# Performance work log

Measured on AMD Instinct MI355X. Metric: run time of the kernel, lower is better.

## Reference

```python
import jax, jax.numpy as jnp
import numpy as np

B, NV, NP, D, K = 8, 2048, 4096, 64, 8  # shapes per batch, vtx/pts counts, feat dim, num_interp
NEG = -1e9


def _unit(x):
    return x / jnp.clip(jnp.linalg.norm(x, axis=-1, keepdims=True), 1e-12)


def _gather(v, idx):
    # v: [B, N, C], idx: [B, Q, K] -> [B, Q, K, C]
    return jax.vmap(lambda a, i: a[i])(v, idx)


def setup_inputs() -> dict:
    key = jax.random.key(0)
    k1, k2, k3, k4, k5 = jax.random.split(key, 5)
    return {
        "vtx": jax.random.normal(k1, (B * NV, 3), jnp.float32),
        "pts": jax.random.normal(k2, (B * NP, 3), jnp.float32),
        "vtx_feature": jax.random.normal(k3, (B * NV, D), jnp.float32),
        "pts_feature": jax.random.normal(k4, (B * NP, D), jnp.float32),
        "vismask_logits": jax.random.normal(k5, (B * NV, 1), jnp.float32),
    }


def reference(vtx, pts, vtx_feature, pts_feature, vismask_logits):
    # --- per-batch min-max normalization of sigmoid(vismask) (serial loop in torch) ---
    vm = jax.nn.sigmoid(vismask_logits).reshape(B, NV, 1)
    vmin = vm.min(axis=1, keepdims=True)
    vmax = vm.max(axis=1, keepdims=True)
    vm = (vm - vmin) / (vmax - vmin)

    vtxb = vtx.reshape(B, NV, 3)
    ptsb = pts.reshape(B, NP, 3)
    vf = vtx_feature.reshape(B, NV, D)
    pf = pts_feature.reshape(B, NP, D)

    # --- cosine KNN: for each vtx, k nearest pts by cosine similarity ---
    sim = jnp.einsum('bnd,bmd->bnm', _unit(vf), _unit(pf))  # [B,NV,NP]
    _, idx = jax.lax.top_k(sim, K)                           # [B,NV,K]

    nbr_pts = _gather(ptsb, idx)                             # [B,NV,K,3]
    nbr_pf = _gather(pf, idx)                                # [B,NV,K,D]
    euclid = nbr_pts - vtxb[:, :, None, :]
    # raw (unnormalized) dot product, weighted by vismask of the query vertex
    fsim = jnp.sum(nbr_pf * vf[:, :, None, :], axis=-1, keepdims=True) * vm[:, :, None, :]
    # scatter_add over assign_index[0] == sum over the K grouped neighbors
    flow_init = jnp.sum(euclid * fsim, axis=2) / jnp.sum(fsim, axis=2)  # [B,NV,3]

    # --- interpolate flow at invisible vertices from visible ones (2nd cosine KNN) ---
    vis = vm >= 0.5                                          # [B,NV,1]
    vfn = _unit(vf)
    sim2 = jnp.einsum('bnd,bmd->bnm', vfn, vfn)              # [B,NV,NV]
    sim2 = jnp.where(vis[:, :, 0][:, None, :], sim2, NEG)    # keys restricted to visible vtx
    _, idx2 = jax.lax.top_k(sim2, K)                         # [B,NV,K]

    nbr_vf = _gather(vf, idx2)                               # [B,NV,K,D]
    nbr_flow = _gather(flow_init, idx2)                      # [B,NV,K,3]
    fsim2 = jnp.sum(nbr_vf * vf[:, :, None, :], axis=-1, keepdims=True)
    invis_flow = jnp.sum(nbr_flow * fsim2, axis=2) / jnp.sum(fsim2, axis=2)

    flow = jnp.where(vis, flow_init, invis_flow)             # flow_init[invis] = invis_flow
    l1_points = jnp.concatenate([flow, vm], axis=-1)         # [B,NV,4]
    return l1_points.reshape(B * NV, 4)
```

## Files before the change

kernel.cpp:

```cpp
#include <hip/hip_runtime.h>
#include <math.h>

#define BB 8
#define NVV 2048
#define NPP 4096
#define DD 64
#define NQ (BB * NVV)
#define QT (NQ / 16)
#define NC1 2
#define NC2 2

typedef __attribute__((ext_vector_type(8))) short short8;
typedef __attribute__((ext_vector_type(8))) unsigned short ushort8;
typedef __attribute__((ext_vector_type(4))) float f32x4;


__device__ __forceinline__ unsigned short bf16rn(float x) {
  unsigned u = __float_as_uint(x);
  return (unsigned short)((u + 0x7FFFu + ((u >> 16) & 1u)) >> 16);
}
__device__ __forceinline__ float bf2f(unsigned short h) {
  return __uint_as_float(((unsigned)h) << 16);
}

__device__ __forceinline__ void net8(unsigned* a, unsigned v) {
#pragma unroll
  for (int k = 0; k < 7; k++) {
    unsigned r;
    asm("v_med3_u32 %0, %1, %2, %3" : "=v"(r) : "v"(v), "v"(a[k]), "v"(a[k + 1]));
    a[k] = r;
  }
  a[7] = a[7] > v ? a[7] : v;
}

__device__ __forceinline__ void ins8(float* tv, int* ti, float v, int id) {
  bool c1 = v > tv[1], c2 = v > tv[2], c3 = v > tv[3];
  bool c4 = v > tv[4], c5 = v > tv[5], c6 = v > tv[6], c7 = v > tv[7];
  tv[0] = c1 ? tv[1] : v;                ti[0] = c1 ? ti[1] : id;
  tv[1] = c2 ? tv[2] : (c1 ? v : tv[1]); ti[1] = c2 ? ti[2] : (c1 ? id : ti[1]);
  tv[2] = c3 ? tv[3] : (c2 ? v : tv[2]); ti[2] = c3 ? ti[3] : (c2 ? id : ti[2]);
  tv[3] = c4 ? tv[4] : (c3 ? v : tv[3]); ti[3] = c4 ? ti[4] : (c3 ? id : ti[3]);
  tv[4] = c5 ? tv[5] : (c4 ? v : tv[4]); ti[4] = c5 ? ti[5] : (c4 ? id : ti[4]);
  tv[5] = c6 ? tv[6] : (c5 ? v : tv[5]); ti[5] = c6 ? ti[6] : (c5 ? id : ti[5]);
  tv[6] = c7 ? tv[7] : (c6 ? v : tv[6]); ti[6] = c7 ? ti[7] : (c6 ? id : ti[6]);
  tv[7] = c7 ? v : tv[7];                ti[7] = c7 ? id : ti[7];
}

__global__ __launch_bounds__(256) void k_prep(const float* __restrict__ logits,
                                              const float* __restrict__ vf,
                                              const float* __restrict__ pf,
                                              float* __restrict__ vm,
                                              float* __restrict__ inv_vf_s,
                                              float* __restrict__ inv_pf_s,
                                              unsigned short* __restrict__ vfh,
                                              unsigned short* __restrict__ vfl,
                                              unsigned short* __restrict__ pfh,
                                              unsigned short* __restrict__ pfl,
                                              float* __restrict__ out) {
  int bid = blockIdx.x, t = threadIdx.x;
  if (bid < BB) {
    int b = bid;
    __shared__ float smn[4], smx[4];
    float vals[8];
    float mn = 1e30f, mx = -1e30f;
#pragma unroll
    for (int i = 0; i < 8; i++) {
      float x = logits[b * NVV + t + i * 256];
      float s = 1.0f / (1.0f + expf(-x));
      vals[i] = s;
      mn = fminf(mn, s);
      mx = fmaxf(mx, s);
    }
    for (int o = 32; o; o >>= 1) {
      mn = fminf(mn, __shfl_xor(mn, o, 64));
      mx = fmaxf(mx, __shfl_xor(mx, o, 64));
    }
    int w = t >> 6;
    if ((t & 63) == 0) { smn[w] = mn; smx[w] = mx; }
    __syncthreads();
    mn = fminf(fminf(smn[0], smn[1]), fminf(smn[2], smn[3]));
    mx = fmaxf(fmaxf(smx[0], smx[1]), fmaxf(smx[2], smx[3]));
    float range = mx - mn;
#pragma unroll
    for (int i = 0; i < 8; i++) {
      float v = (vals[i] - mn) / range;
      int g = b * NVV + t + i * 256;
      vm[g] = v;
      out[g * 4 + 3] = v;
    }
  } else {
    int tile_g = (bid - BB) * 4 + (t >> 6);
    int lane = t & 63, c = lane & 15, quad = (lane >> 4) & 3;
    const float* src;
    unsigned short *dh, *dl;
    float* ginv;
    int tile;
    if (tile_g < QT) { tile = tile_g; src = vf; dh = vfh; dl = vfl; ginv = inv_vf_s; }
    else { tile = tile_g - QT; src = pf; dh = pfh; dl = pfl; ginv = inv_pf_s; }
    int row = tile * 16 + c;
    const float* rp = src + (size_t)row * DD + quad * 8;
    float4 a0 = *(const float4*)(rp);
    float4 b0 = *(const float4*)(rp + 4);
    float4 a1 = *(const float4*)(rp + 32);
    float4 b1 = *(const float4*)(rp + 36);
    float xs[16] = {a0.x, a0.y, a0.z, a0.w, b0.x, b0.y, b0.z, b0.w,
                    a1.x, a1.y, a1.z, a1.w, b1.x, b1.y, b1.z, b1.w};
    float ss = 0.f;
#pragma unroll
    for (int j = 0; j < 16; j++) ss = fmaf(xs[j], xs[j], ss);
    ss += __shfl_xor(ss, 16, 64);
    ss += __shfl_xor(ss, 32, 64);
    float inv = 1.0f / fmaxf(sqrtf(ss), 1e-12f);
    if (quad == 0) ginv[row] = 16384.0f * inv;
    ushort8 h, l;
    size_t s0 = (size_t)tile * 128 + lane;
#pragma unroll
    for (int j = 0; j < 8; j++) {
      float xn = xs[j] * inv;
      unsigned short hj = bf16rn(xn);
      h[j] = hj;
      l[j] = bf16rn(xn - bf2f(hj));
    }
    *(ushort8*)(dh + s0 * 8) = h;
    *(ushort8*)(dl + s0 * 8) = l;
#pragma unroll
    for (int j = 0; j < 8; j++) {
      float xn = xs[8 + j] * inv;
      unsigned short hj = bf16rn(xn);
      h[j] = hj;
      l[j] = bf16rn(xn - bf2f(hj));
    }
    *(ushort8*)(dh + (s0 + 64) * 8) = h;
    *(ushort8*)(dl + (s0 + 64) * 8) = l;
  }
}

__global__ __launch_bounds__(256)
void k_knn(const unsigned short* __restrict__ vfh, const unsigned short* __restrict__ vfl,
           const unsigned short* __restrict__ pfh, const unsigned short* __restrict__ pfl,
           const float* __restrict__ vm,
           unsigned* __restrict__ pc1, unsigned* __restrict__ pc2) {
  int wid = (blockIdx.x * 256 + threadIdx.x) >> 6;
  int lane = threadIdx.x & 63, col = lane & 15, quad = lane >> 4;

  const unsigned short *KH, *KL;
  const float* mask;
  unsigned* PC;
  int qt_g, bt0, row0, ckb, ntiles;
  if (wid < QT * NC1) {
    int ck = wid & 1;
    qt_g = wid >> 1;
    int batch = qt_g >> 7;
    KH = pfh; KL = pfl;
    mask = nullptr;
    ntiles = 128;
    bt0 = batch * 256 + ck * 128;
    PC = pc1;
    row0 = ck * 8; ckb = ck * 128;
  } else {
    int w = wid - QT * NC1;
    int ck = w & 1;
    qt_g = w >> 1;
    int batch = qt_g >> 7;
    KH = vfh; KL = vfl;
    mask = vm + batch * NVV;
    ntiles = 64;
    bt0 = batch * 128 + ck * 64;
    PC = pc2;
    row0 = ck * 8; ckb = ck * 64;
  }

  size_t ab = (size_t)qt_g * 1024 + lane * 8;
  short8 qh0 = *(const short8*)(vfh + ab);
  short8 qh1 = *(const short8*)(vfh + ab + 512);
  short8 ql0 = *(const short8*)(vfl + ab);
  short8 ql1 = *(const short8*)(vfl + ab + 512);
  asm volatile("" : "+a"(qh0), "+a"(qh1), "+a"(ql0), "+a"(ql1));

  unsigned tv[8];
#pragma unroll
  for (int k = 0; k < 8; k++) tv[k] = 0u;

#pragma unroll 2
  for (int kt = 0; kt < ntiles; kt++) {
    size_t bo = (size_t)(bt0 + kt) * 1024 + lane * 8;
    short8 kh0 = *(const short8*)(KH + bo);
    short8 kh1 = *(const short8*)(KH + bo + 512);
    short8 kl0 = *(const short8*)(KL + bo);
    short8 kl1 = *(const short8*)(KL + bo + 512);
    int base16 = (ckb + kt) * 16;
    f32x4 c = {0.f, 0.f, 0.f, 0.f};
    c = __builtin_amdgcn_mfma_f32_16x16x32_bf16(kh0, qh0, c, 0, 0, 0);
    c = __builtin_amdgcn_mfma_f32_16x16x32_bf16(kh1, qh1, c, 0, 0, 0);
    c = __builtin_amdgcn_mfma_f32_16x16x32_bf16(kh0, ql0, c, 0, 0, 0);
    c = __builtin_amdgcn_mfma_f32_16x16x32_bf16(kh1, ql1, c, 0, 0, 0);
    c = __builtin_amdgcn_mfma_f32_16x16x32_bf16(kl0, qh0, c, 0, 0, 0);
    c = __builtin_amdgcn_mfma_f32_16x16x32_bf16(kl1, qh1, c, 0, 0, 0);
    float4 mv;
    if (mask) mv = *(const float4*)(mask + base16 + quad * 4);
#pragma unroll
    for (int r = 0; r < 4; r++) {
      unsigned u = (unsigned)fmaxf(fmaf(c[r], 520000.0f, 520000.0f), 0.0f);
      unsigned pk = (u << 12) | (unsigned)(base16 + quad * 4 + r);
      if (mask) {
        float mr = (r == 0) ? mv.x : (r == 1) ? mv.y : (r == 2) ? mv.z : mv.w;
        pk = (mr >= 0.5f) ? pk : 0u;
      }
      net8(tv, pk);
    }
  }

#pragma unroll
  for (int m = 16; m <= 32; m <<= 1) {
    unsigned ov[8];
#pragma unroll
    for (int k = 0; k < 8; k++) ov[k] = (unsigned)__shfl_xor((int)tv[k], m, 64);
#pragma unroll
    for (int k = 7; k >= 0; k--) net8(tv, ov[k]);
  }

  if (quad == 0) {
    int q = qt_g * 16 + col;
#pragma unroll
    for (int k = 0; k < 8; k++)
      PC[(size_t)(row0 + k) * NQ + q] = tv[k];
  }
}

__device__ __forceinline__ float dot64(const float4* __restrict__ a,
                                       const float4* __restrict__ b) {
  float a0 = 0.f, a1 = 0.f, a2 = 0.f, a3 = 0.f;
#pragma unroll
  for (int c = 0; c < 16; c++) {
    float4 x = a[c], y = b[c];
    a0 = fmaf(x.x, y.x, a0);
    a1 = fmaf(x.y, y.y, a1);
    a2 = fmaf(x.z, y.z, a2);
    a3 = fmaf(x.w, y.w, a3);
  }
  return (a0 + a1) + (a2 + a3);
}

__global__ __launch_bounds__(256) void k_merge_flow(const unsigned* __restrict__ pc,
                                                    const float* __restrict__ vf,
                                                    const float* __restrict__ pf,
                                                    const float* __restrict__ pts,
                                                    const float* __restrict__ vtx,
                                                    const float* __restrict__ inv_pf_s,
                                                    float* __restrict__ flow_ws,
                                                    float* __restrict__ out) {
  int T = blockIdx.x * 256 + threadIdx.x;
  int q = T >> 4, c = T & 15, batch = q >> 11;
  const float4* qp = (const float4*)(vf + (size_t)q * DD);
  float tv[8];
  int ti[8];
#pragma unroll
  for (int k = 0; k < 8; k++) { tv[k] = -3.0e38f; ti[k] = 0; }
  {
    unsigned pk = pc[(size_t)c * NQ + q];
    int id = (int)(pk & 0xFFFu);
    int prow = batch * NPP + id;
    float s = dot64(qp, (const float4*)(pf + (size_t)prow * DD)) *
              inv_pf_s[prow] * 6.103515625e-5f;
    ins8(tv, ti, s, id);
  }
#pragma unroll
  for (int m = 1; m <= 8; m <<= 1) {
    float ov[8];
    int oi[8];
#pragma unroll
    for (int k = 0; k < 8; k++) {
      ov[k] = __shfl_xor(tv[k], m, 64);
      oi[k] = __shfl_xor(ti[k], m, 64);
    }
#pragma unroll
    for (int k = 7; k >= 0; k--)
      if (ov[k] > tv[0]) ins8(tv, ti, ov[k], oi[k]);
  }
  int id = ti[0];
  float sv = tv[0];
#pragma unroll
  for (int k = 1; k < 8; k++) {
    id = (c == k) ? ti[k] : id;
    sv = (c == k) ? tv[k] : sv;
  }

  float ax = 0.f, ay = 0.f, az = 0.f, den = 0.f;
  if (c < 8) {
    int prow = batch * NPP + id;
    float w = sv * 16384.0f / inv_pf_s[prow];
    ax = (pts[prow * 3 + 0] - vtx[q * 3 + 0]) * w;
    ay = (pts[prow * 3 + 1] - vtx[q * 3 + 1]) * w;
    az = (pts[prow * 3 + 2] - vtx[q * 3 + 2]) * w;
    den = w;
  }
#pragma unroll
  for (int m = 1; m <= 8; m <<= 1) {
    ax += __shfl_xor(ax, m, 64);
    ay += __shfl_xor(ay, m, 64);
    az += __shfl_xor(az, m, 64);
    den += __shfl_xor(den, m, 64);
  }
  if (c == 0) {
    float fx = ax / den, fy = ay / den, fz = az / den;
    flow_ws[q * 4 + 0] = fx;
    flow_ws[q * 4 + 1] = fy;
    flow_ws[q * 4 + 2] = fz;
    out[q * 4 + 0] = fx;
    out[q * 4 + 1] = fy;
    out[q * 4 + 2] = fz;
  }
}

__global__ __launch_bounds__(256) void k_merge_final(const unsigned* __restrict__ pc,
                                                     const float* __restrict__ vf,
                                                     const float* __restrict__ vm,
                                                     const float* __restrict__ inv_vf_s,
                                                     const float* __restrict__ flow_ws,
                                                     float* __restrict__ out) {
  int T = blockIdx.x * 256 + threadIdx.x;
  int q = T >> 4, c = T & 15, batch = q >> 11;
  if (vm[q] >= 0.5f) return;
  const float4* qp = (const float4*)(vf + (size_t)q * DD);
  float tv[8];
  int ti[8];
#pragma unroll
  for (int k = 0; k < 8; k++) { tv[k] = -3.0e38f; ti[k] = 0; }
  {
    unsigned pk = pc[(size_t)c * NQ + q];
    if (pk > 0xFFFu) {
      int id = (int)(pk & 0xFFFu);
      int krow = batch * NVV + id;
      float s = dot64(qp, (const float4*)(vf + (size_t)krow * DD)) *
                inv_vf_s[krow] * 6.103515625e-5f;
      ins8(tv, ti, s, id);
    }
  }
#pragma unroll
  for (int m = 1; m <= 8; m <<= 1) {
    float ov[8];
    int oi[8];
#pragma unroll
    for (int k = 0; k < 8; k++) {
      ov[k] = __shfl_xor(tv[k], m, 64);
      oi[k] = __shfl_xor(ti[k], m, 64);
    }
#pragma unroll
    for (int k = 7; k >= 0; k--)
      if (ov[k] > tv[0]) ins8(tv, ti, ov[k], oi[k]);
  }
  int id = ti[0];
  float sv = tv[0];
#pragma unroll
  for (int k = 1; k < 8; k++) {
    id = (c == k) ? ti[k] : id;
    sv = (c == k) ? tv[k] : sv;
  }

  float ax = 0.f, ay = 0.f, az = 0.f, den = 0.f;
  if (c < 8) {
    int krow = batch * NVV + id;
    float w = sv * 16384.0f / inv_vf_s[krow];
    ax = flow_ws[krow * 4 + 0] * w;
    ay = flow_ws[krow * 4 + 1] * w;
    az = flow_ws[krow * 4 + 2] * w;
    den = w;
  }
#pragma unroll
  for (int m = 1; m <= 8; m <<= 1) {
    ax += __shfl_xor(ax, m, 64);
    ay += __shfl_xor(ay, m, 64);
    az += __shfl_xor(az, m, 64);
    den += __shfl_xor(den, m, 64);
  }
  if (c == 0) {
    out[q * 4 + 0] = ax / den;
    out[q * 4 + 1] = ay / den;
    out[q * 4 + 2] = az / den;
  }
}

extern "C" void kernel_launch(void* const* d_in, const int* in_sizes, int n_in,
                              void* d_out, int out_size, void* d_ws, size_t ws_size,
                              hipStream_t stream) {
  const float* vtx = (const float*)d_in[0];
  const float* pts = (const float*)d_in[1];
  const float* vf = (const float*)d_in[2];
  const float* pf = (const float*)d_in[3];
  const float* lg = (const float*)d_in[4];
  float* out = (float*)d_out;
  float* ws = (float*)d_ws;

  float* vm = ws;
  float* inv_vf_s = ws + 16384;
  float* inv_pf_s = ws + 32768;
  float* flow = ws + 65536;
  unsigned* pc1 = (unsigned*)(ws + 131072);
  unsigned* pc2 = (unsigned*)(ws + 393216);
  unsigned short* vfh = (unsigned short*)(ws + 655360);
  unsigned short* vfl = (unsigned short*)(ws + 1179648);
  unsigned short* pfh = (unsigned short*)(ws + 1703936);
  unsigned short* pfl = (unsigned short*)(ws + 2752512);

  k_prep<<<BB + 768, 256, 0, stream>>>(lg, vf, pf, vm, inv_vf_s, inv_pf_s,
                                       vfh, vfl, pfh, pfl, out);
  k_knn<<<(QT * NC1 + QT * NC2) / 4, 256, 0, stream>>>(vfh, vfl, pfh, pfl,
                                                       vm, pc1, pc2);
  k_merge_flow<<<NQ * 16 / 256, 256, 0, stream>>>(pc1, vf, pf, pts, vtx,
                                                  inv_pf_s, flow, out);
  k_merge_final<<<NQ * 16 / 256, 256, 0, stream>>>(pc2, vf, vm, inv_vf_s, flow, out);
}
```

Before: 178.9 us.

## Split KNN key chunks across wave pairs and remap blocks per XCD

Each (query tile, key chunk) unit is now processed by two waves, each scanning half of the key tiles. The two partial top-8 lists are merged through shared memory after a block barrier. Block indices are also remapped so consecutive query tiles land on the same XCD, which should improve L2 reuse of key data. This doubles the wave count to shorten per-wave serial MFMA and sort chains, at the cost of an extra LDS merge and a __syncthreads.

Result: no change. 179.9 us (+0.6%).

```diff
diff --git a/kernel.cpp b/kernel.cpp
--- a/kernel.cpp
+++ b/kernel.cpp
@@ -140,34 +140,43 @@
            const unsigned short* __restrict__ pfh, const unsigned short* __restrict__ pfl,
            const float* __restrict__ vm,
            unsigned* __restrict__ pc1, unsigned* __restrict__ pc2) {
-  int wid = (blockIdx.x * 256 + threadIdx.x) >> 6;
-  int lane = threadIdx.x & 63, col = lane & 15, quad = lane >> 4;
+  __shared__ unsigned mg[2][16][8];
+
+  int p = blockIdx.x;
+  int tid = threadIdx.x;
+  int pairid = tid >> 7;
+  int wv = (tid >> 6) & 1;
+  int lane = tid & 63, col = lane & 15, quad = lane >> 4;
+
+  bool knn1 = p < 1024;
+  int q8 = knn1 ? p : (p - 1024);
+  int xcd = q8 & 7, idx = q8 >> 3;
+  int lb = xcd * 128 + idx;
+  int unit = lb * 2 + pairid;
+  int ck = unit & 1;
+  int qt_g = unit >> 1;
+  int batch = qt_g >> 7;
 
   const unsigned short *KH, *KL;
   const float* mask;
   unsigned* PC;
-  int qt_g, bt0, row0, ckb, ntiles;
-  if (wid < QT * NC1) {
-    int ck = wid & 1;
-    qt_g = wid >> 1;
-    int batch = qt_g >> 7;
+  int bt0, tilebase, half, row0;
+  if (knn1) {
     KH = pfh; KL = pfl;
     mask = nullptr;
-    ntiles = 128;
-    bt0 = batch * 256 + ck * 128;
+    half = 64;
+    bt0 = batch * 256 + ck * 128 + wv * 64;
+    tilebase = ck * 128 + wv * 64;
     PC = pc1;
-    row0 = ck * 8; ckb = ck * 128;
+    row0 = ck * 8;
   } else {
-    int w = wid - QT * NC1;
-    int ck = w & 1;
-    qt_g = w >> 1;
-    int batch = qt_g >> 7;
     KH = vfh; KL = vfl;
     mask = vm + batch * NVV;
-    ntiles = 64;
-    bt0 = batch * 128 + ck * 64;
+    half = 32;
+    bt0 = batch * 128 + ck * 64 + wv * 32;
+    tilebase = ck * 64 + wv * 32;
     PC = pc2;
-    row0 = ck * 8; ckb = ck * 64;
+    row0 = ck * 8;
   }
 
   size_t ab = (size_t)qt_g * 1024 + lane * 8;
@@ -182,13 +191,13 @@
   for (int k = 0; k < 8; k++) tv[k] = 0u;
 
 #pragma unroll 2
-  for (int kt = 0; kt < ntiles; kt++) {
+  for (int kt = 0; kt < half; kt++) {
     size_t bo = (size_t)(bt0 + kt) * 1024 + lane * 8;
     short8 kh0 = *(const short8*)(KH + bo);
     short8 kh1 = *(const short8*)(KH + bo + 512);
     short8 kl0 = *(const short8*)(KL + bo);
     short8 kl1 = *(const short8*)(KL + bo + 512);
-    int base16 = (ckb + kt) * 16;
+    int base16 = (tilebase + kt) * 16;
     f32x4 c = {0.f, 0.f, 0.f, 0.f};
     c = __builtin_amdgcn_mfma_f32_16x16x32_bf16(kh0, qh0, c, 0, 0, 0);
     c = __builtin_amdgcn_mfma_f32_16x16x32_bf16(kh1, qh1, c, 0, 0, 0);
@@ -219,8 +228,15 @@
     for (int k = 7; k >= 0; k--) net8(tv, ov[k]);
   }
 
-  if (quad == 0) {
-    int q = qt_g * 16 + col;
+  if (wv == 1 && lane < 16) {
+#pragma unroll
+    for (int k = 0; k < 8; k++) mg[pairid][lane][k] = tv[k];
+  }
+  __syncthreads();
+  if (wv == 0 && lane < 16) {
+#pragma unroll
+    for (int k = 0; k < 8; k++) net8(tv, mg[pairid][lane][k]);
+    int q = qt_g * 16 + lane;
 #pragma unroll
     for (int k = 0; k < 8; k++)
       PC[(size_t)(row0 + k) * NQ + q] = tv[k];
@@ -404,8 +420,7 @@
 
   k_prep<<<BB + 768, 256, 0, stream>>>(lg, vf, pf, vm, inv_vf_s, inv_pf_s,
                                        vfh, vfl, pfh, pfl, out);
-  k_knn<<<(QT * NC1 + QT * NC2) / 4, 256, 0, stream>>>(vfh, vfl, pfh, pfl,
-                                                       vm, pc1, pc2);
+  k_knn<<<2048, 256, 0, stream>>>(vfh, vfl, pfh, pfl, vm, pc1, pc2);
   k_merge_flow<<<NQ * 16 / 256, 256, 0, stream>>>(pc1, vf, pf, pts, vtx,
                                                   inv_pf_s, flow, out);
   k_merge_final<<<NQ * 16 / 256, 256, 0, stream>>>(pc2, vf, vm, inv_vf_s, flow, out);
```

## Restructure KNN kernel: one block per query tile, split keys across waves, XCD-aware mapping

Applied to the files above, without the earlier changes.

Each block now owns one 16-query tile and runs both KNN passes (points, then visible vertices). The four waves each scan a quarter of the keys, and the two half-chunk partial top-8 lists are merged through shared memory. Block indices are mapped so that each XCD handles a single batch, which should improve L2 reuse of that batch's key data. This gives finer work granularity and load balance, at the cost of two block syncs and a shared-memory merge.

Measured after the change: 174.9 us. 1.02x faster.

```diff
diff --git a/kernel.cpp b/kernel.cpp
--- a/kernel.cpp
+++ b/kernel.cpp
@@ -140,35 +140,15 @@
            const unsigned short* __restrict__ pfh, const unsigned short* __restrict__ pfl,
            const float* __restrict__ vm,
            unsigned* __restrict__ pc1, unsigned* __restrict__ pc2) {
-  int wid = (blockIdx.x * 256 + threadIdx.x) >> 6;
+  __shared__ unsigned mg[2][2][16][8];
+
+  int p = blockIdx.x;
+  int xcd = p & 7, j = p >> 3;
+  int qt_g = xcd * 128 + j;
+  int batch = xcd;
+  int w = (int)threadIdx.x >> 6;
+  int ck = w >> 1, hf = w & 1;
   int lane = threadIdx.x & 63, col = lane & 15, quad = lane >> 4;
-
-  const unsigned short *KH, *KL;
-  const float* mask;
-  unsigned* PC;
-  int qt_g, bt0, row0, ckb, ntiles;
-  if (wid < QT * NC1) {
-    int ck = wid & 1;
-    qt_g = wid >> 1;
-    int batch = qt_g >> 7;
-    KH = pfh; KL = pfl;
-    mask = nullptr;
-    ntiles = 128;
-    bt0 = batch * 256 + ck * 128;
-    PC = pc1;
-    row0 = ck * 8; ckb = ck * 128;
-  } else {
-    int w = wid - QT * NC1;
-    int ck = w & 1;
-    qt_g = w >> 1;
-    int batch = qt_g >> 7;
-    KH = vfh; KL = vfl;
-    mask = vm + batch * NVV;
-    ntiles = 64;
-    bt0 = batch * 128 + ck * 64;
-    PC = pc2;
-    row0 = ck * 8; ckb = ck * 64;
-  }
 
   size_t ab = (size_t)qt_g * 1024 + lane * 8;
   short8 qh0 = *(const short8*)(vfh + ab);
@@ -178,38 +158,89 @@
   asm volatile("" : "+a"(qh0), "+a"(qh1), "+a"(ql0), "+a"(ql1));
 
   unsigned tv[8];
+
 #pragma unroll
   for (int k = 0; k < 8; k++) tv[k] = 0u;
-
+  {
+    int bt0 = batch * 256 + ck * 128 + hf * 64;
+    int tb = ck * 128 + hf * 64;
 #pragma unroll 2
-  for (int kt = 0; kt < ntiles; kt++) {
-    size_t bo = (size_t)(bt0 + kt) * 1024 + lane * 8;
-    short8 kh0 = *(const short8*)(KH + bo);
-    short8 kh1 = *(const short8*)(KH + bo + 512);
-    short8 kl0 = *(const short8*)(KL + bo);
-    short8 kl1 = *(const short8*)(KL + bo + 512);
-    int base16 = (ckb + kt) * 16;
-    f32x4 c = {0.f, 0.f, 0.f, 0.f};
-    c = __builtin_amdgcn_mfma_f32_16x16x32_bf16(kh0, qh0, c, 0, 0, 0);
-    c = __builtin_amdgcn_mfma_f32_16x16x32_bf16(kh1, qh1, c, 0, 0, 0);
-    c = __builtin_amdgcn_mfma_f32_16x16x32_bf16(kh0, ql0, c, 0, 0, 0);
-    c = __builtin_amdgcn_mfma_f32_16x16x32_bf16(kh1, ql1, c, 0, 0, 0);
-    c = __builtin_amdgcn_mfma_f32_16x16x32_bf16(kl0, qh0, c, 0, 0, 0);
-    c = __builtin_amdgcn_mfma_f32_16x16x32_bf16(kl1, qh1, c, 0, 0, 0);
-    float4 mv;
-    if (mask) mv = *(const float4*)(mask + base16 + quad * 4);
-#pragma unroll
-    for (int r = 0; r < 4; r++) {
-      unsigned u = (unsigned)fmaxf(fmaf(c[r], 520000.0f, 520000.0f), 0.0f);
-      unsigned pk = (u << 12) | (unsigned)(base16 + quad * 4 + r);
-      if (mask) {
+    for (int kt = 0; kt < 64; kt++) {
+      size_t bo = (size_t)(bt0 + kt) * 1024 + lane * 8;
+      short8 kh0 = *(const short8*)(pfh + bo);
+      short8 kh1 = *(const short8*)(pfh + bo + 512);
+      short8 kl0 = *(const short8*)(pfl + bo);
+      short8 kl1 = *(const short8*)(pfl + bo + 512);
+      int base16 = (tb + kt) * 16;
+      f32x4 c = {0.f, 0.f, 0.f, 0.f};
+      c = __builtin_amdgcn_mfma_f32_16x16x32_bf16(kh0, qh0, c, 0, 0, 0);
+      c = __builtin_amdgcn_mfma_f32_16x16x32_bf16(kh1, qh1, c, 0, 0, 0);
+      c = __builtin_amdgcn_mfma_f32_16x16x32_bf16(kh0, ql0, c, 0, 0, 0);
+      c = __builtin_amdgcn_mfma_f32_16x16x32_bf16(kh1, ql1, c, 0, 0, 0);
+      c = __builtin_amdgcn_mfma_f32_16x16x32_bf16(kl0, qh0, c, 0, 0, 0);
+      c = __builtin_amdgcn_mfma_f32_16x16x32_bf16(kl1, qh1, c, 0, 0, 0);
+#pragma unroll
+      for (int r = 0; r < 4; r++) {
+        unsigned u = (unsigned)fmaxf(fmaf(c[r], 520000.0f, 520000.0f), 0.0f);
+        unsigned pk = (u << 12) | (unsigned)(base16 + quad * 4 + r);
+        net8(tv, pk);
+      }
+    }
+  }
+#pragma unroll
+  for (int m = 16; m <= 32; m <<= 1) {
+    unsigned ov[8];
+#pragma unroll
+    for (int k = 0; k < 8; k++) ov[k] = (unsigned)__shfl_xor((int)tv[k], m, 64);
+#pragma unroll
+    for (int k = 7; k >= 0; k--) net8(tv, ov[k]);
+  }
+  if (hf == 1 && quad == 0) {
+#pragma unroll
+    for (int k = 0; k < 8; k++) mg[0][ck][col][k] = tv[k];
+  }
+  __syncthreads();
+  if (hf == 0 && quad == 0) {
+#pragma unroll
+    for (int k = 0; k < 8; k++) net8(tv, mg[0][ck][col][k]);
+    int q = qt_g * 16 + col;
+#pragma unroll
+    for (int k = 0; k < 8; k++)
+      pc1[(size_t)(ck * 8 + k) * NQ + q] = tv[k];
+  }
+
+#pragma unroll
+  for (int k = 0; k < 8; k++) tv[k] = 0u;
+  {
+    const float* mask = vm + batch * NVV;
+    int bt0 = batch * 128 + ck * 64 + hf * 32;
+    int tb = ck * 64 + hf * 32;
+#pragma unroll 2
+    for (int kt = 0; kt < 32; kt++) {
+      size_t bo = (size_t)(bt0 + kt) * 1024 + lane * 8;
+      short8 kh0 = *(const short8*)(vfh + bo);
+      short8 kh1 = *(const short8*)(vfh + bo + 512);
+      short8 kl0 = *(const short8*)(vfl + bo);
+      short8 kl1 = *(const short8*)(vfl + bo + 512);
+      int base16 = (tb + kt) * 16;
+      f32x4 c = {0.f, 0.f, 0.f, 0.f};
+      c = __builtin_amdgcn_mfma_f32_16x16x32_bf16(kh0, qh0, c, 0, 0, 0);
+      c = __builtin_amdgcn_mfma_f32_16x16x32_bf16(kh1, qh1, c, 0, 0, 0);
+      c = __builtin_amdgcn_mfma_f32_16x16x32_bf16(kh0, ql0, c, 0, 0, 0);
+      c = __builtin_amdgcn_mfma_f32_16x16x32_bf16(kh1, ql1, c, 0, 0, 0);
+      c = __builtin_amdgcn_mfma_f32_16x16x32_bf16(kl0, qh0, c, 0, 0, 0);
+      c = __builtin_amdgcn_mfma_f32_16x16x32_bf16(kl1, qh1, c, 0, 0, 0);
+      float4 mv = *(const float4*)(mask + base16 + quad * 4);
+#pragma unroll
+      for (int r = 0; r < 4; r++) {
+        unsigned u = (unsigned)fmaxf(fmaf(c[r], 520000.0f, 520000.0f), 0.0f);
+        unsigned pk = (u << 12) | (unsigned)(base16 + quad * 4 + r);
         float mr = (r == 0) ? mv.x : (r == 1) ? mv.y : (r == 2) ? mv.z : mv.w;
         pk = (mr >= 0.5f) ? pk : 0u;
+        net8(tv, pk);
       }
-      net8(tv, pk);
-    }
-  }
-
+    }
+  }
 #pragma unroll
   for (int m = 16; m <= 32; m <<= 1) {
     unsigned ov[8];
@@ -218,12 +249,18 @@
 #pragma unroll
     for (int k = 7; k >= 0; k--) net8(tv, ov[k]);
   }
-
-  if (quad == 0) {
+  if (hf == 1 && quad == 0) {
+#pragma unroll
+    for (int k = 0; k < 8; k++) mg[1][ck][col][k] = tv[k];
+  }
+  __syncthreads();
+  if (hf == 0 && quad == 0) {
+#pragma unroll
+    for (int k = 0; k < 8; k++) net8(tv, mg[1][ck][col][k]);
     int q = qt_g * 16 + col;
 #pragma unroll
     for (int k = 0; k < 8; k++)
-      PC[(size_t)(row0 + k) * NQ + q] = tv[k];
+      pc2[(size_t)(ck * 8 + k) * NQ + q] = tv[k];
   }
 }
 
@@ -404,8 +441,7 @@
 
   k_prep<<<BB + 768, 256, 0, stream>>>(lg, vf, pf, vm, inv_vf_s, inv_pf_s,
                                        vfh, vfl, pfh, pfl, out);
-  k_knn<<<(QT * NC1 + QT * NC2) / 4, 256, 0, stream>>>(vfh, vfl, pfh, pfl,
-                                                       vm, pc1, pc2);
+  k_knn<<<1024, 256, 0, stream>>>(vfh, vfl, pfh, pfl, vm, pc1, pc2);
   k_merge_flow<<<NQ * 16 / 256, 256, 0, stream>>>(pc1, vf, pf, pts, vtx,
                                                   inv_pf_s, flow, out);
   k_merge_final<<<NQ * 16 / 256, 256, 0, stream>>>(pc2, vf, vm, inv_vf_s, flow, out);
```
